# Kernel tuning notes

Measured on AMD Instinct MI355X. Metric: run time of the kernel, lower is better.

The kernel has to match this reference:

```python
import jax, jax.numpy as jnp
import numpy as np

N_NODES = 100000


def _gcn_norm(edge_index, num_nodes):
    # PyG GCNConv default: add self-loops, symmetric normalization
    row, col = edge_index[0], edge_index[1]
    loop = jnp.arange(num_nodes, dtype=edge_index.dtype)
    row = jnp.concatenate([row, loop])
    col = jnp.concatenate([col, loop])
    ones = jnp.ones(col.shape[0], dtype=jnp.float32)
    deg = jax.ops.segment_sum(ones, col, num_segments=num_nodes)
    dinv = jnp.where(deg > 0, jax.lax.rsqrt(deg), 0.0)
    norm = dinv[row] * dinv[col]  # [E + N]
    return row, col, norm


def _gcn_conv(x, W, b, row, col, norm, num_nodes):
    h = x @ W                               # [N, out] linear transform first
    msg = h[row] * norm[:, None]            # gather + edge-wise scale
    out = jax.ops.segment_sum(msg, col, num_segments=num_nodes)  # scatter-add
    return out + b


def setup_inputs() -> dict:
    key = jax.random.key(0)
    k1, k2, k3, k4 = jax.random.split(key, 4)
    E = 1600000
    x = jax.random.normal(k1, (N_NODES, 128), dtype=jnp.float32)
    edge_index = jax.random.randint(k2, (2, E), 0, N_NODES, dtype=jnp.int64)
    W1 = jax.random.normal(k3, (128, 128), dtype=jnp.float32) * (1.0 / np.sqrt(128))
    b1 = jnp.zeros((128,), dtype=jnp.float32)
    W2 = jax.random.normal(k4, (128, 64), dtype=jnp.float32) * (1.0 / np.sqrt(128))
    b2 = jnp.zeros((64,), dtype=jnp.float32)
    return {"x": x, "edge_index": edge_index, "W1": W1, "b1": b1, "W2": W2, "b2": b2}


def reference(x, edge_index, W1, b1, W2, b2):
    num_nodes = x.shape[0]
    row, col, norm = _gcn_norm(edge_index, num_nodes)
    h = _gcn_conv(x, W1, b1, row, col, norm, num_nodes)
    h = jax.nn.relu(h)
    out = _gcn_conv(h, W2, b2, row, col, norm, num_nodes)
    return out
```

## Files before the change

kernel.cpp:

```cpp
#include <hip/hip_runtime.h>
#include <hip/hip_bf16.h>

typedef unsigned short u16;
typedef unsigned char u8;
typedef short bf16x8 __attribute__((ext_vector_type(8)));
typedef float f32x4 __attribute__((ext_vector_type(4)));

__device__ __forceinline__ float bflo(unsigned u) { return __uint_as_float(u << 16); }
__device__ __forceinline__ float bfhi(unsigned u) { return __uint_as_float(u & 0xffff0000u); }
__device__ __forceinline__ u16 f2bf(float f) {
    unsigned u = __float_as_uint(f);
    return (u16)((u + 0x7fffu + ((u >> 16) & 1u)) >> 16);
}

#define CHUNK 2048
#define BN 512

#define PK_RMASK 0x7fffffu

__global__ __launch_bounds__(256) void hist_prep_kernel(const int* __restrict__ cols,
                                                        unsigned* __restrict__ hist,
                                                        int E, int nbuckets, int nblocksA,
                                                        const float* __restrict__ W1,
                                                        const float* __restrict__ W2,
                                                        u16* __restrict__ WT1,
                                                        u16* __restrict__ WT2) {
    int blk = blockIdx.x;
    if (blk >= nblocksA) {
        int t = (blk - nblocksA) * 256 + threadIdx.x;
        if (t < 128 * 128) {
            int n = t >> 7, k = t & 127;
            WT1[n * 128 + k] = f2bf(W1[k * 128 + n]);
        } else if (t < 128 * 128 + 64 * 128) {
            int i = t - 128 * 128;
            int n = i >> 7, k = i & 127;
            WT2[n * 128 + k] = f2bf(W2[k * 64 + n]);
        }
        return;
    }
    __shared__ unsigned h[256];
    int t = threadIdx.x;
    h[t] = 0;
    __syncthreads();
    int base = blk * CHUNK;
#pragma unroll
    for (int j = 0; j < CHUNK / 256; j++) {
        int i = base + j * 256 + t;
        if (i < E) atomicAdd(&h[((unsigned)cols[i]) >> 9], 1u);
    }
    __syncthreads();
    if (t < nbuckets) hist[blk * nbuckets + t] = h[t];
}

__global__ __launch_bounds__(256) void scanA1_kernel(unsigned* __restrict__ hist,
                                                     unsigned* __restrict__ totals,
                                                     int nblocksA, int nbuckets) {
    __shared__ unsigned s[256];
    int t = threadIdx.x, b = blockIdx.x;
    unsigned v[4];
    unsigned sum = 0;
#pragma unroll
    for (int k = 0; k < 4; k++) {
        int blk = t * 4 + k;
        v[k] = (blk < nblocksA) ? hist[(size_t)blk * nbuckets + b] : 0u;
        sum += v[k];
    }
    s[t] = sum;
    __syncthreads();
    unsigned val = sum;
    for (int off = 1; off < 256; off <<= 1) {
        unsigned x = (t >= off) ? s[t - off] : 0u;
        __syncthreads();
        s[t] += x;
        __syncthreads();
    }
    unsigned ex = s[t] - val;
#pragma unroll
    for (int k = 0; k < 4; k++) {
        int blk = t * 4 + k;
        if (blk < nblocksA) hist[(size_t)blk * nbuckets + b] = ex;
        ex += v[k];
    }
    if (t == 255) totals[b] = s[255];
}

__global__ __launch_bounds__(256) void scanA2_kernel(const unsigned* __restrict__ totals,
                                                     unsigned* __restrict__ bucketbase,
                                                     int nbuckets) {
    __shared__ unsigned s[256];
    int t = threadIdx.x;
    unsigned val = (t < nbuckets) ? totals[t] : 0u;
    s[t] = val;
    __syncthreads();
    for (int off = 1; off < 256; off <<= 1) {
        unsigned v = (t >= off) ? s[t - off] : 0u;
        __syncthreads();
        s[t] += v;
        __syncthreads();
    }
    unsigned ex = s[t] - val;
    if (t < nbuckets) bucketbase[t] = ex;
    if (t == nbuckets - 1) bucketbase[nbuckets] = ex + val;
}

__global__ __launch_bounds__(256) void scatterA_kernel(const int* __restrict__ rows,
                                                       const int* __restrict__ cols,
                                                       const unsigned* __restrict__ hist,
                                                       const unsigned* __restrict__ bucketbase,
                                                       unsigned* __restrict__ binned,
                                                       int E, int nbuckets) {
    __shared__ unsigned sp[CHUNK];
    __shared__ u8 spg[CHUNK];
    __shared__ unsigned lstart[256];
    __shared__ unsigned lcur[256];
    __shared__ unsigned gbase[256];
    int t = threadIdx.x, blk = blockIdx.x;
    int base = blk * CHUNK;
    int cnt = min(CHUNK, E - base);

    lcur[t] = 0;
    __syncthreads();
    for (int i = t; i < cnt; i += 256)
        atomicAdd(&lcur[((unsigned)cols[base + i]) >> 9], 1u);
    __syncthreads();
    unsigned val = lcur[t];
    lstart[t] = val;
    __syncthreads();
    for (int off = 1; off < 256; off <<= 1) {
        unsigned v = (t >= off) ? lstart[t - off] : 0u;
        __syncthreads();
        lstart[t] += v;
        __syncthreads();
    }
    unsigned ex = lstart[t] - val;
    __syncthreads();
    lstart[t] = ex;
    lcur[t] = ex;
    if (t < nbuckets) gbase[t] = bucketbase[t] + hist[(size_t)blk * nbuckets + t];
    __syncthreads();
    for (int i = t; i < cnt; i += 256) {
        unsigned c = (unsigned)cols[base + i];
        unsigned r = (unsigned)rows[base + i];
        unsigned g = c >> 9;
        unsigned pos = atomicAdd(&lcur[g], 1u);
        sp[pos] = r | ((c & 511u) << 23);
        spg[pos] = (u8)g;
    }
    __syncthreads();
    for (int i = t; i < cnt; i += 256) {
        unsigned pk = sp[i];
        unsigned g = spg[i];
        binned[gbase[g] + (unsigned)i - lstart[g]] = pk;
    }
}

__global__ __launch_bounds__(256) void binB_kernel(const unsigned* __restrict__ binned,
                                                   const unsigned* __restrict__ bucketbase,
                                                   int* __restrict__ rowptr,
                                                   float* __restrict__ dinv,
                                                   int* __restrict__ srcidx,
                                                   int N, int E, int nbuckets) {
    __shared__ unsigned cnt[BN + 1];
    __shared__ unsigned sc[BN + 1];
    __shared__ unsigned ps[256];
    int t = threadIdx.x, b = blockIdx.x;
    int lo = b << 9;
    int nn = min(BN, N - lo);
    unsigned s = bucketbase[b], e = bucketbase[b + 1];

    cnt[t] = 0;
    cnt[t + 256] = 0;
    if (t == 0) cnt[BN] = 0;
    __syncthreads();
    for (unsigned i = s + t; i < e; i += 256)
        atomicAdd(&cnt[binned[i] >> 23], 1u);
    __syncthreads();

    unsigned a0 = cnt[2 * t], a1 = cnt[2 * t + 1];
    ps[t] = a0 + a1;
    __syncthreads();
    unsigned val = ps[t];
    for (int off = 1; off < 256; off <<= 1) {
        unsigned v = (t >= off) ? ps[t - off] : 0u;
        __syncthreads();
        ps[t] += v;
        __syncthreads();
    }
    unsigned ex = ps[t] - val;
    sc[2 * t] = ex;
    sc[2 * t + 1] = ex + a0;
    if (t == 255) sc[BN] = ex + val;
    __syncthreads();

    for (int n = t; n < nn; n += 256) {
        unsigned rp = s + sc[n];
        rowptr[lo + n] = (int)rp;
        dinv[lo + n] = rsqrtf((float)(sc[n + 1] - sc[n]) + 1.0f);
        cnt[n] = rp;
    }
    if (b == nbuckets - 1 && t == 0) rowptr[N] = E;
    __syncthreads();

    for (unsigned i = s + t; i < e; i += 256) {
        unsigned pk = binned[i];
        unsigned slot = atomicAdd(&cnt[pk >> 23], 1u);
        srcidx[slot] = (int)(pk & PK_RMASK);
    }
}

template <int NOUT, bool IN_BF16>
__global__ __launch_bounds__(256) void gemm_mfma(const void* __restrict__ Xv,
                                                 const u16* __restrict__ WT,
                                                 const float* __restrict__ dinv,
                                                 u16* __restrict__ OutH, int nrows) {
    constexpr int LDK = 136;
    __shared__ u16 sX[64 * LDK];
    __shared__ u16 sW[NOUT * LDK];

    const int t = threadIdx.x;
    const int wv = t >> 6, lane = t & 63;
    const int m = lane & 15, q = lane >> 4;
    const int row0 = blockIdx.x * 64;

    for (int idx = t; idx < NOUT * 16; idx += 256) {
        int n = idx >> 4, c = idx & 15;
        *((uint4*)&sW[n * LDK + c * 8]) = ((const uint4*)WT)[idx];
    }
    if (IN_BF16) {
        const u16* X = (const u16*)Xv;
        for (int idx = t; idx < 64 * 16; idx += 256) {
            int r = idx >> 4, c = idx & 15;
            int gr = row0 + r;
            uint4 v = make_uint4(0u, 0u, 0u, 0u);
            if (gr < nrows) v = ((const uint4*)X)[(size_t)gr * 16 + c];
            *((uint4*)&sX[r * LDK + c * 8]) = v;
        }
    } else {
        const float* X = (const float*)Xv;
        for (int idx = t; idx < 64 * 32; idx += 256) {
            int r = idx >> 5, c = idx & 31;
            int gr = row0 + r;
            float4 v = make_float4(0.f, 0.f, 0.f, 0.f);
            if (gr < nrows) v = ((const float4*)X)[(size_t)gr * 32 + c];
            uint2 o;
            o.x = (unsigned)f2bf(v.x) | ((unsigned)f2bf(v.y) << 16);
            o.y = (unsigned)f2bf(v.z) | ((unsigned)f2bf(v.w) << 16);
            *((uint2*)&sX[r * LDK + c * 4]) = o;
        }
    }
    __syncthreads();

    f32x4 acc[NOUT / 16];
#pragma unroll
    for (int i = 0; i < NOUT / 16; i++) acc[i] = (f32x4){0.f, 0.f, 0.f, 0.f};

#pragma unroll
    for (int ks = 0; ks < 4; ks++) {
        const int k0 = ks * 32 + q * 8;
        bf16x8 a = *((const bf16x8*)&sX[(wv * 16 + m) * LDK + k0]);
#pragma unroll
        for (int nt = 0; nt < NOUT / 16; nt++) {
            bf16x8 b = *((const bf16x8*)&sW[(nt * 16 + m) * LDK + k0]);
            acc[nt] = __builtin_amdgcn_mfma_f32_16x16x32_bf16(a, b, acc[nt], 0, 0, 0);
        }
    }

#pragma unroll
    for (int r = 0; r < 4; r++) {
        int gi = row0 + wv * 16 + q * 4 + r;
        if (gi < nrows) {
            float dv = dinv[gi];
#pragma unroll
            for (int nt = 0; nt < NOUT / 16; nt++) {
                OutH[(size_t)gi * NOUT + nt * 16 + m] = f2bf(acc[nt][r] * dv);
            }
        }
    }
}

__global__ __launch_bounds__(256) void agg1_gemm2(const int* __restrict__ rowptr,
                                                  const int* __restrict__ srcidx,
                                                  const u16* __restrict__ hs,
                                                  const float* __restrict__ dinv,
                                                  const float* __restrict__ bias,
                                                  const u16* __restrict__ WT2,
                                                  u16* __restrict__ h2s, int N) {
    constexpr int WPN = 16;
    constexpr int LDK = 136;
    __shared__ u16 sO[16 * LDK];
    __shared__ u16 sW[64 * LDK];

    const int t = threadIdx.x;
    const int node_l = t / WPN;
    const int fl = t % WPN;
    const int node = blockIdx.x * 16 + node_l;
    const bool valid = node < N;

    for (int idx = t; idx < 64 * 16; idx += 256) {
        int n = idx >> 4, c = idx & 15;
        *((uint4*)&sW[n * LDK + c * 8]) = ((const uint4*)WT2)[idx];
    }

    const uint4* h128 = (const uint4*)hs;
    float a[8];
#pragma unroll
    for (int j = 0; j < 8; j++) a[j] = 0.f;

    if (valid) {
        int start = rowptr[node], end = rowptr[node + 1];
        {
            uint4 v = h128[(size_t)node * WPN + fl];
            a[0] = bflo(v.x); a[1] = bfhi(v.x); a[2] = bflo(v.y); a[3] = bfhi(v.y);
            a[4] = bflo(v.z); a[5] = bfhi(v.z); a[6] = bflo(v.w); a[7] = bfhi(v.w);
        }
        int nfull = (end - start) >> 3;
        int i = start;
        int r[8], r2[8];
        if (nfull > 0) {
#pragma unroll
            for (int j = 0; j < 8; j++) r[j] = srcidx[i + j];
        }
        for (int b = 0; b < nfull; b++) {
            uint4 u[8];
#pragma unroll
            for (int j = 0; j < 8; j++) u[j] = h128[(size_t)r[j] * WPN + fl];
            if (b + 1 < nfull) {
#pragma unroll
                for (int j = 0; j < 8; j++) r2[j] = srcidx[i + 8 + j];
            }
#pragma unroll
            for (int j = 0; j < 8; j++) {
                a[0] += bflo(u[j].x); a[1] += bfhi(u[j].x);
                a[2] += bflo(u[j].y); a[3] += bfhi(u[j].y);
                a[4] += bflo(u[j].z); a[5] += bfhi(u[j].z);
                a[6] += bflo(u[j].w); a[7] += bfhi(u[j].w);
            }
#pragma unroll
            for (int j = 0; j < 8; j++) r[j] = r2[j];
            i += 8;
        }
        if (i + 4 <= end) {
            int rr[4];
#pragma unroll
            for (int j = 0; j < 4; j++) rr[j] = srcidx[i + j];
            uint4 u[4];
#pragma unroll
            for (int j = 0; j < 4; j++) u[j] = h128[(size_t)rr[j] * WPN + fl];
#pragma unroll
            for (int j = 0; j < 4; j++) {
                a[0] += bflo(u[j].x); a[1] += bfhi(u[j].x);
                a[2] += bflo(u[j].y); a[3] += bfhi(u[j].y);
                a[4] += bflo(u[j].z); a[5] += bfhi(u[j].z);
                a[6] += bflo(u[j].w); a[7] += bfhi(u[j].w);
            }
            i += 4;
        }
        for (; i < end; ++i) {
            uint4 u = h128[(size_t)srcidx[i] * WPN + fl];
            a[0] += bflo(u.x); a[1] += bfhi(u.x);
            a[2] += bflo(u.y); a[3] += bfhi(u.y);
            a[4] += bflo(u.z); a[5] += bfhi(u.z);
            a[6] += bflo(u.w); a[7] += bfhi(u.w);
        }
    }

    float dv = valid ? dinv[node] : 0.f;
    float4 bv0 = ((const float4*)bias)[2 * fl];
    float4 bv1 = ((const float4*)bias)[2 * fl + 1];
    float o[8];
    o[0] = fmaxf(dv * a[0] + bv0.x, 0.f); o[1] = fmaxf(dv * a[1] + bv0.y, 0.f);
    o[2] = fmaxf(dv * a[2] + bv0.z, 0.f); o[3] = fmaxf(dv * a[3] + bv0.w, 0.f);
    o[4] = fmaxf(dv * a[4] + bv1.x, 0.f); o[5] = fmaxf(dv * a[5] + bv1.y, 0.f);
    o[6] = fmaxf(dv * a[6] + bv1.z, 0.f); o[7] = fmaxf(dv * a[7] + bv1.w, 0.f);
    uint4 w;
    w.x = (unsigned)f2bf(o[0]) | ((unsigned)f2bf(o[1]) << 16);
    w.y = (unsigned)f2bf(o[2]) | ((unsigned)f2bf(o[3]) << 16);
    w.z = (unsigned)f2bf(o[4]) | ((unsigned)f2bf(o[5]) << 16);
    w.w = (unsigned)f2bf(o[6]) | ((unsigned)f2bf(o[7]) << 16);
    *((uint4*)&sO[node_l * LDK + fl * 8]) = w;
    __syncthreads();

    const int wv = t >> 6, lane = t & 63;
    const int m = lane & 15, q = lane >> 4;
    f32x4 acc = (f32x4){0.f, 0.f, 0.f, 0.f};
#pragma unroll
    for (int ks = 0; ks < 4; ks++) {
        const int k0 = ks * 32 + q * 8;
        bf16x8 af = *((const bf16x8*)&sO[m * LDK + k0]);
        bf16x8 bf = *((const bf16x8*)&sW[(wv * 16 + m) * LDK + k0]);
        acc = __builtin_amdgcn_mfma_f32_16x16x32_bf16(af, bf, acc, 0, 0, 0);
    }
#pragma unroll
    for (int r = 0; r < 4; r++) {
        int gi = blockIdx.x * 16 + q * 4 + r;
        if (gi < N) {
            float dvv = dinv[gi];
            h2s[(size_t)gi * 64 + wv * 16 + m] = f2bf(acc[r] * dvv);
        }
    }
}

template <int NH, bool RELU, bool OUT_BF16>
__global__ __launch_bounds__(256) void aggregate(const int* __restrict__ rowptr,
                                                 const int* __restrict__ srcidx,
                                                 const u16* __restrict__ hs,
                                                 const float* __restrict__ dinv,
                                                 const float* __restrict__ bias,
                                                 void* __restrict__ outv, int N) {
    constexpr int WPN = NH / 8;
    int tid = blockIdx.x * 256 + threadIdx.x;
    int node = tid / WPN;
    int fl = tid % WPN;
    if (node >= N) return;

    const uint4* h128 = (const uint4*)hs;
    int start = rowptr[node], end = rowptr[node + 1];

    float a[8];
    {
        uint4 v = h128[(size_t)node * WPN + fl];
        a[0] = bflo(v.x); a[1] = bfhi(v.x); a[2] = bflo(v.y); a[3] = bfhi(v.y);
        a[4] = bflo(v.z); a[5] = bfhi(v.z); a[6] = bflo(v.w); a[7] = bfhi(v.w);
    }

    int nfull = (end - start) >> 3;
    int i = start;
    int r[8], r2[8];
    if (nfull > 0) {
#pragma unroll
        for (int j = 0; j < 8; j++) r[j] = srcidx[i + j];
    }
    for (int b = 0; b < nfull; b++) {
        uint4 u[8];
#pragma unroll
        for (int j = 0; j < 8; j++) u[j] = h128[(size_t)r[j] * WPN + fl];
        if (b + 1 < nfull) {
#pragma unroll
            for (int j = 0; j < 8; j++) r2[j] = srcidx[i + 8 + j];
        }
#pragma unroll
        for (int j = 0; j < 8; j++) {
            a[0] += bflo(u[j].x); a[1] += bfhi(u[j].x);
            a[2] += bflo(u[j].y); a[3] += bfhi(u[j].y);
            a[4] += bflo(u[j].z); a[5] += bfhi(u[j].z);
            a[6] += bflo(u[j].w); a[7] += bfhi(u[j].w);
        }
#pragma unroll
        for (int j = 0; j < 8; j++) r[j] = r2[j];
        i += 8;
    }
    if (i + 4 <= end) {
        int rr[4];
#pragma unroll
        for (int j = 0; j < 4; j++) rr[j] = srcidx[i + j];
        uint4 u[4];
#pragma unroll
        for (int j = 0; j < 4; j++) u[j] = h128[(size_t)rr[j] * WPN + fl];
#pragma unroll
        for (int j = 0; j < 4; j++) {
            a[0] += bflo(u[j].x); a[1] += bfhi(u[j].x);
            a[2] += bflo(u[j].y); a[3] += bfhi(u[j].y);
            a[4] += bflo(u[j].z); a[5] += bfhi(u[j].z);
            a[6] += bflo(u[j].w); a[7] += bfhi(u[j].w);
        }
        i += 4;
    }
    for (; i < end; ++i) {
        uint4 u = h128[(size_t)srcidx[i] * WPN + fl];
        a[0] += bflo(u.x); a[1] += bfhi(u.x);
        a[2] += bflo(u.y); a[3] += bfhi(u.y);
        a[4] += bflo(u.z); a[5] += bfhi(u.z);
        a[6] += bflo(u.w); a[7] += bfhi(u.w);
    }

    float dv = dinv[node];
    float4 bv0 = ((const float4*)bias)[2 * fl];
    float4 bv1 = ((const float4*)bias)[2 * fl + 1];
    float o[8];
    o[0] = dv * a[0] + bv0.x; o[1] = dv * a[1] + bv0.y;
    o[2] = dv * a[2] + bv0.z; o[3] = dv * a[3] + bv0.w;
    o[4] = dv * a[4] + bv1.x; o[5] = dv * a[5] + bv1.y;
    o[6] = dv * a[6] + bv1.z; o[7] = dv * a[7] + bv1.w;
    if (RELU) {
#pragma unroll
        for (int j = 0; j < 8; j++) o[j] = fmaxf(o[j], 0.f);
    }
    if (OUT_BF16) {
        uint4 w;
        w.x = (unsigned)f2bf(o[0]) | ((unsigned)f2bf(o[1]) << 16);
        w.y = (unsigned)f2bf(o[2]) | ((unsigned)f2bf(o[3]) << 16);
        w.z = (unsigned)f2bf(o[4]) | ((unsigned)f2bf(o[5]) << 16);
        w.w = (unsigned)f2bf(o[6]) | ((unsigned)f2bf(o[7]) << 16);
        ((uint4*)outv)[tid] = w;
    } else {
        ((float4*)outv)[2 * tid] = make_float4(o[0], o[1], o[2], o[3]);
        ((float4*)outv)[2 * tid + 1] = make_float4(o[4], o[5], o[6], o[7]);
    }
}

extern "C" void kernel_launch(void* const* d_in, const int* in_sizes, int n_in,
                              void* d_out, int out_size, void* d_ws, size_t ws_size,
                              hipStream_t stream) {
    const float* x  = (const float*)d_in[0];
    const int*   ei = (const int*)d_in[1];
    const float* W1 = (const float*)d_in[2];
    const float* b1 = (const float*)d_in[3];
    const float* W2 = (const float*)d_in[4];
    const float* b2 = (const float*)d_in[5];

    const int N = in_sizes[0] / 128;
    const int E = in_sizes[1] / 2;
    const int* rows = ei;
    const int* cols = ei + E;

    const int nbuckets = (N + BN - 1) / BN;
    const int nblocksA = (E + CHUNK - 1) / CHUNK;

    char* ws = (char*)d_ws;
    size_t off = 0;
    auto alloc = [&](size_t bytes) -> void* {
        void* p = ws + off;
        off = (off + bytes + 1023) & ~(size_t)1023;
        return p;
    };
    unsigned* hist       = (unsigned*)alloc((size_t)nbuckets * nblocksA * 4);
    unsigned* totals     = (unsigned*)alloc(256 * 4);
    unsigned* bucketbase = (unsigned*)alloc((size_t)(nbuckets + 1) * 4);
    unsigned* binned     = (unsigned*)alloc((size_t)E * 4);
    int*      rowptr     = (int*)alloc((size_t)(N + 1) * 4);
    float*    dinv       = (float*)alloc((size_t)N * 4);
    int*      srcidx     = (int*)alloc((size_t)E * 4);
    u16*      WT1        = (u16*)alloc((size_t)128 * 128 * 2);
    u16*      WT2        = (u16*)alloc((size_t)64 * 128 * 2);
    u16*      h1s        = (u16*)alloc((size_t)N * 128 * 2);
    u16*      h2s        = (u16*)alloc((size_t)N * 64 * 2);

    hist_prep_kernel<<<nblocksA + 96, 256, 0, stream>>>(cols, hist, E, nbuckets, nblocksA,
                                                        W1, W2, WT1, WT2);
    scanA1_kernel<<<nbuckets, 256, 0, stream>>>(hist, totals, nblocksA, nbuckets);
    scanA2_kernel<<<1, 256, 0, stream>>>(totals, bucketbase, nbuckets);
    scatterA_kernel<<<nblocksA, 256, 0, stream>>>(rows, cols, hist, bucketbase, binned, E, nbuckets);
    binB_kernel<<<nbuckets, 256, 0, stream>>>(binned, bucketbase, rowptr, dinv, srcidx, N, E, nbuckets);

    gemm_mfma<128, false><<<(N + 63) / 64, 256, 0, stream>>>(x, WT1, dinv, h1s, N);

    agg1_gemm2<<<(N + 15) / 16, 256, 0, stream>>>(rowptr, srcidx, h1s, dinv, b1, WT2, h2s, N);

    aggregate<64, false, false><<<(N * 8 + 255) / 256, 256, 0, stream>>>(
        rowptr, srcidx, h2s, dinv, b2, d_out, N);
}
```

Baseline: 261.4 us.

## Halve CSR bucket width and double GEMM row tile per block

Node buckets for the two-pass CSR build shrink from 512 to 256 nodes, which doubles the bucket count (about 391). Histogram, scan and scatter kernels are adapted to handle up to 512 buckets, and binB now works one node per thread. This gives more, smaller binB blocks for better parallelism and smaller per-block sorting work. Separately, the first GEMM now handles 128 rows per block with two accumulator sets per wave, reusing the W fragments loaded from LDS, at the cost of more LDS and registers.

```diff
diff --git a/kernel.cpp b/kernel.cpp
--- a/kernel.cpp
+++ b/kernel.cpp
@@ -14,7 +14,8 @@
 }
 
 #define CHUNK 2048
-#define BN 512
+#define BN 256
+#define BSH 8
 
 #define PK_RMASK 0x7fffffu
 
@@ -38,18 +39,19 @@
         }
         return;
     }
-    __shared__ unsigned h[256];
+    __shared__ unsigned h[512];
     int t = threadIdx.x;
     h[t] = 0;
+    h[t + 256] = 0;
     __syncthreads();
     int base = blk * CHUNK;
 #pragma unroll
     for (int j = 0; j < CHUNK / 256; j++) {
         int i = base + j * 256 + t;
-        if (i < E) atomicAdd(&h[((unsigned)cols[i]) >> 9], 1u);
-    }
-    __syncthreads();
-    if (t < nbuckets) hist[blk * nbuckets + t] = h[t];
+        if (i < E) atomicAdd(&h[((unsigned)cols[i]) >> BSH], 1u);
+    }
+    __syncthreads();
+    for (int k = t; k < nbuckets; k += 256) hist[(size_t)blk * nbuckets + k] = h[k];
 }
 
 __global__ __launch_bounds__(256) void scanA1_kernel(unsigned* __restrict__ hist,
@@ -89,18 +91,31 @@
                                                      int nbuckets) {
     __shared__ unsigned s[256];
     int t = threadIdx.x;
-    unsigned val = (t < nbuckets) ? totals[t] : 0u;
-    s[t] = val;
-    __syncthreads();
+    unsigned v[2];
+    unsigned sum = 0;
+#pragma unroll
+    for (int k = 0; k < 2; k++) {
+        int i = 2 * t + k;
+        v[k] = (i < nbuckets) ? totals[i] : 0u;
+        sum += v[k];
+    }
+    s[t] = sum;
+    __syncthreads();
+    unsigned val = sum;
     for (int off = 1; off < 256; off <<= 1) {
-        unsigned v = (t >= off) ? s[t - off] : 0u;
-        __syncthreads();
-        s[t] += v;
+        unsigned x = (t >= off) ? s[t - off] : 0u;
+        __syncthreads();
+        s[t] += x;
         __syncthreads();
     }
     unsigned ex = s[t] - val;
-    if (t < nbuckets) bucketbase[t] = ex;
-    if (t == nbuckets - 1) bucketbase[nbuckets] = ex + val;
+#pragma unroll
+    for (int k = 0; k < 2; k++) {
+        int i = 2 * t + k;
+        if (i < nbuckets) bucketbase[i] = ex;
+        ex += v[k];
+    }
+    if (t == 255) bucketbase[nbuckets] = s[255];
 }
 
 __global__ __launch_bounds__(256) void scatterA_kernel(const int* __restrict__ rows,
@@ -110,41 +125,46 @@
                                                        unsigned* __restrict__ binned,
                                                        int E, int nbuckets) {
     __shared__ unsigned sp[CHUNK];
-    __shared__ u8 spg[CHUNK];
-    __shared__ unsigned lstart[256];
-    __shared__ unsigned lcur[256];
-    __shared__ unsigned gbase[256];
+    __shared__ u16 spg[CHUNK];
+    __shared__ unsigned lstart[512];
+    __shared__ unsigned lcur[512];
+    __shared__ unsigned gbase[512];
+    __shared__ unsigned ps[256];
     int t = threadIdx.x, blk = blockIdx.x;
     int base = blk * CHUNK;
     int cnt = min(CHUNK, E - base);
 
     lcur[t] = 0;
+    lcur[t + 256] = 0;
     __syncthreads();
     for (int i = t; i < cnt; i += 256)
-        atomicAdd(&lcur[((unsigned)cols[base + i]) >> 9], 1u);
-    __syncthreads();
-    unsigned val = lcur[t];
-    lstart[t] = val;
-    __syncthreads();
+        atomicAdd(&lcur[((unsigned)cols[base + i]) >> BSH], 1u);
+    __syncthreads();
+    unsigned v0 = lcur[2 * t], v1 = lcur[2 * t + 1];
+    ps[t] = v0 + v1;
+    __syncthreads();
+    unsigned val = ps[t];
     for (int off = 1; off < 256; off <<= 1) {
-        unsigned v = (t >= off) ? lstart[t - off] : 0u;
-        __syncthreads();
-        lstart[t] += v;
-        __syncthreads();
-    }
-    unsigned ex = lstart[t] - val;
-    __syncthreads();
-    lstart[t] = ex;
-    lcur[t] = ex;
-    if (t < nbuckets) gbase[t] = bucketbase[t] + hist[(size_t)blk * nbuckets + t];
+        unsigned x = (t >= off) ? ps[t - off] : 0u;
+        __syncthreads();
+        ps[t] += x;
+        __syncthreads();
+    }
+    unsigned ex = ps[t] - val;
+    lstart[2 * t] = ex;
+    lstart[2 * t + 1] = ex + v0;
+    lcur[2 * t] = ex;
+    lcur[2 * t + 1] = ex + v0;
+    for (int k = t; k < nbuckets; k += 256)
+        gbase[k] = bucketbase[k] + hist[(size_t)blk * nbuckets + k];
     __syncthreads();
     for (int i = t; i < cnt; i += 256) {
         unsigned c = (unsigned)cols[base + i];
         unsigned r = (unsigned)rows[base + i];
-        unsigned g = c >> 9;
+        unsigned g = c >> BSH;
         unsigned pos = atomicAdd(&lcur[g], 1u);
-        sp[pos] = r | ((c & 511u) << 23);
-        spg[pos] = (u8)g;
+        sp[pos] = r | ((c & 255u) << 23);
+        spg[pos] = (u16)g;
     }
     __syncthreads();
     for (int i = t; i < cnt; i += 256) {
@@ -164,39 +184,35 @@
     __shared__ unsigned sc[BN + 1];
     __shared__ unsigned ps[256];
     int t = threadIdx.x, b = blockIdx.x;
-    int lo = b << 9;
+    int lo = b << BSH;
     int nn = min(BN, N - lo);
     unsigned s = bucketbase[b], e = bucketbase[b + 1];
 
     cnt[t] = 0;
-    cnt[t + 256] = 0;
     if (t == 0) cnt[BN] = 0;
     __syncthreads();
     for (unsigned i = s + t; i < e; i += 256)
         atomicAdd(&cnt[binned[i] >> 23], 1u);
     __syncthreads();
 
-    unsigned a0 = cnt[2 * t], a1 = cnt[2 * t + 1];
-    ps[t] = a0 + a1;
-    __syncthreads();
-    unsigned val = ps[t];
+    unsigned val = cnt[t];
+    ps[t] = val;
+    __syncthreads();
     for (int off = 1; off < 256; off <<= 1) {
         unsigned v = (t >= off) ? ps[t - off] : 0u;
         __syncthreads();
         ps[t] += v;
         __syncthreads();
     }
-    unsigned ex = ps[t] - val;
-    sc[2 * t] = ex;
-    sc[2 * t + 1] = ex + a0;
-    if (t == 255) sc[BN] = ex + val;
-    __syncthreads();
-
-    for (int n = t; n < nn; n += 256) {
-        unsigned rp = s + sc[n];
-        rowptr[lo + n] = (int)rp;
-        dinv[lo + n] = rsqrtf((float)(sc[n + 1] - sc[n]) + 1.0f);
-        cnt[n] = rp;
+    sc[t] = ps[t] - val;
+    if (t == 255) sc[BN] = ps[255];
+    __syncthreads();
+
+    if (t < nn) {
+        unsigned rp = s + sc[t];
+        rowptr[lo + t] = (int)rp;
+        dinv[lo + t] = rsqrtf((float)(sc[t + 1] - sc[t]) + 1.0f);
+        cnt[t] = rp;
     }
     if (b == nbuckets - 1 && t == 0) rowptr[N] = E;
     __syncthreads();
@@ -214,13 +230,13 @@
                                                  const float* __restrict__ dinv,
                                                  u16* __restrict__ OutH, int nrows) {
     constexpr int LDK = 136;
-    __shared__ u16 sX[64 * LDK];
+    __shared__ u16 sX[128 * LDK];
     __shared__ u16 sW[NOUT * LDK];
 
     const int t = threadIdx.x;
     const int wv = t >> 6, lane = t & 63;
     const int m = lane & 15, q = lane >> 4;
-    const int row0 = blockIdx.x * 64;
+    const int row0 = blockIdx.x * 128;
 
     for (int idx = t; idx < NOUT * 16; idx += 256) {
         int n = idx >> 4, c = idx & 15;
@@ -228,7 +244,7 @@
     }
     if (IN_BF16) {
         const u16* X = (const u16*)Xv;
-        for (int idx = t; idx < 64 * 16; idx += 256) {
+        for (int idx = t; idx < 128 * 16; idx += 256) {
             int r = idx >> 4, c = idx & 15;
             int gr = row0 + r;
             uint4 v = make_uint4(0u, 0u, 0u, 0u);
@@ -237,7 +253,7 @@
         }
     } else {
         const float* X = (const float*)Xv;
-        for (int idx = t; idx < 64 * 32; idx += 256) {
+        for (int idx = t; idx < 128 * 32; idx += 256) {
             int r = idx >> 5, c = idx & 31;
             int gr = row0 + r;
             float4 v = make_float4(0.f, 0.f, 0.f, 0.f);
@@ -250,29 +266,42 @@
     }
     __syncthreads();
 
-    f32x4 acc[NOUT / 16];
-#pragma unroll
-    for (int i = 0; i < NOUT / 16; i++) acc[i] = (f32x4){0.f, 0.f, 0.f, 0.f};
+    f32x4 acc0[NOUT / 16], acc1[NOUT / 16];
+#pragma unroll
+    for (int i = 0; i < NOUT / 16; i++) {
+        acc0[i] = (f32x4){0.f, 0.f, 0.f, 0.f};
+        acc1[i] = (f32x4){0.f, 0.f, 0.f, 0.f};
+    }
 
 #pragma unroll
     for (int ks = 0; ks < 4; ks++) {
         const int k0 = ks * 32 + q * 8;
-        bf16x8 a = *((const bf16x8*)&sX[(wv * 16 + m) * LDK + k0]);
+        bf16x8 a0 = *((const bf16x8*)&sX[(wv * 32 + m) * LDK + k0]);
+        bf16x8 a1 = *((const bf16x8*)&sX[(wv * 32 + 16 + m) * LDK + k0]);
 #pragma unroll
         for (int nt = 0; nt < NOUT / 16; nt++) {
             bf16x8 b = *((const bf16x8*)&sW[(nt * 16 + m) * LDK + k0]);
-            acc[nt] = __builtin_amdgcn_mfma_f32_16x16x32_bf16(a, b, acc[nt], 0, 0, 0);
+            acc0[nt] = __builtin_amdgcn_mfma_f32_16x16x32_bf16(a0, b, acc0[nt], 0, 0, 0);
+            acc1[nt] = __builtin_amdgcn_mfma_f32_16x16x32_bf16(a1, b, acc1[nt], 0, 0, 0);
         }
     }
 
 #pragma unroll
     for (int r = 0; r < 4; r++) {
-        int gi = row0 + wv * 16 + q * 4 + r;
+        int gi = row0 + wv * 32 + q * 4 + r;
         if (gi < nrows) {
             float dv = dinv[gi];
 #pragma unroll
             for (int nt = 0; nt < NOUT / 16; nt++) {
-                OutH[(size_t)gi * NOUT + nt * 16 + m] = f2bf(acc[nt][r] * dv);
+                OutH[(size_t)gi * NOUT + nt * 16 + m] = f2bf(acc0[nt][r] * dv);
+            }
+        }
+        int gj = gi + 16;
+        if (gj < nrows) {
+            float dv = dinv[gj];
+#pragma unroll
+            for (int nt = 0; nt < NOUT / 16; nt++) {
+                OutH[(size_t)gj * NOUT + nt * 16 + m] = f2bf(acc1[nt][r] * dv);
             }
         }
     }
@@ -524,7 +553,7 @@
         return p;
     };
     unsigned* hist       = (unsigned*)alloc((size_t)nbuckets * nblocksA * 4);
-    unsigned* totals     = (unsigned*)alloc(256 * 4);
+    unsigned* totals     = (unsigned*)alloc(512 * 4);
     unsigned* bucketbase = (unsigned*)alloc((size_t)(nbuckets + 1) * 4);
     unsigned* binned     = (unsigned*)alloc((size_t)E * 4);
     int*      rowptr     = (int*)alloc((size_t)(N + 1) * 4);
@@ -542,7 +571,7 @@
     scatterA_kernel<<<nblocksA, 256, 0, stream>>>(rows, cols, hist, bucketbase, binned, E, nbuckets);
     binB_kernel<<<nbuckets, 256, 0, stream>>>(binned, bucketbase, rowptr, dinv, srcidx, N, E, nbuckets);
 
-    gemm_mfma<128, false><<<(N + 63) / 64, 256, 0, stream>>>(x, WT1, dinv, h1s, N);
+    gemm_mfma<128, false><<<(N + 127) / 128, 256, 0, stream>>>(x, WT1, dinv, h1s, N);
 
     agg1_gemm2<<<(N + 15) / 16, 256, 0, stream>>>(rowptr, srcidx, h1s, dinv, b1, WT2, h2s, N);
 
```

Result: no change. 264.8 us (+1.3%).
